# Optimization experiments

Hardware: AMD Instinct MI355X
Metric: run time of the kernel (lower is better)

Reference implementation:

```python
import jax, jax.numpy as jnp
import numpy as np

WS = 4      # window_size (RSUT5 default)
SHIFT = 2   # window_size // 2
NH = 8      # num_heads
DIM = 256
H0 = W0 = T0 = 32
B0 = 1


def _ln(x, g, b, eps=1e-5):
    m = x.mean(-1, keepdims=True)
    v = ((x - m) ** 2).mean(-1, keepdims=True)
    return (x - m) / jnp.sqrt(v + eps) * g + b


def _rel_index(ws):
    c = np.stack(np.meshgrid(np.arange(ws), np.arange(ws), np.arange(ws), indexing='ij')).reshape(3, -1)
    r = (c[:, :, None] - c[:, None, :]).transpose(1, 2, 0) + (ws - 1)
    return jnp.asarray((r[..., 0] * (2 * ws - 1) + r[..., 1]) * (2 * ws - 1) + r[..., 2])


def _partition(x, ws):
    B, H, W, T, C = x.shape
    x = x.reshape(B, H // ws, ws, W // ws, ws, T // ws, ws, C)
    return x.transpose(0, 1, 3, 5, 2, 4, 6, 7).reshape(-1, ws ** 3, C)


def _reverse(w, ws, B, H, W, T):
    C = w.shape[-1]
    x = w.reshape(B, H // ws, W // ws, T // ws, ws, ws, ws, C)
    return x.transpose(0, 1, 4, 2, 5, 3, 6, 7).reshape(B, H, W, T, C)


def _attn_mask(H, W, T, ws, ss):
    # static (numpy) replica of Block.createmask; H,W,T divisible by ws here
    img = np.zeros((H, W, T), np.float32)
    sls = (slice(0, -ws), slice(-ws, -ss), slice(-ss, None))
    cnt = 0
    for h in sls:
        for w in sls:
            for t in sls:
                img[h, w, t] = cnt
                cnt += 1
    mw = img.reshape(H // ws, ws, W // ws, ws, T // ws, ws).transpose(0, 2, 4, 1, 3, 5).reshape(-1, ws ** 3)
    d = mw[:, None, :] - mw[:, :, None]
    return jnp.asarray(np.where(d != 0, -100.0, 0.0).astype(np.float32))


def _swin(x, H, W, T, shift, mask, n1g, n1b, qkvw, qkvb, rpb, projw, projb, n2g, n2b, fc1w, fc1b, fc2w, fc2b):
    B, L, C = x.shape
    N = WS ** 3
    hd = C // NH
    shortcut = x
    x = _ln(x, n1g, n1b).reshape(B, H, W, T, C)
    if shift:
        x = jnp.roll(x, (-shift, -shift, -shift), axis=(1, 2, 3))
    xw = _partition(x, WS)                                        # [B*nW, N, C]
    qkv = (xw @ qkvw.T + qkvb).reshape(-1, N, 3, NH, hd).transpose(2, 0, 3, 1, 4)
    q, k, v = qkv[0], qkv[1], qkv[2]                              # [B*nW, NH, N, hd]
    attn = jnp.einsum('bhnd,bhmd->bhnm', q * (hd ** -0.5), k)
    attn = attn + rpb[_rel_index(WS)].transpose(2, 0, 1)[None]    # relative position bias
    if mask is not None:
        nW = mask.shape[0]
        attn = (attn.reshape(B, nW, NH, N, N) + mask[None, :, None]).reshape(-1, NH, N, N)
    attn = jax.nn.softmax(attn, axis=-1)
    out = jnp.einsum('bhnm,bhmd->bhnd', attn, v).transpose(0, 2, 1, 3).reshape(-1, N, C)
    out = out @ projw.T + projb
    x = _reverse(out, WS, B, H, W, T)
    if shift:
        x = jnp.roll(x, (shift, shift, shift), axis=(1, 2, 3))
    x = shortcut + x.reshape(B, L, C)
    h = _ln(x, n2g, n2b)
    h = jax.nn.gelu(h @ fc1w.T + fc1b, approximate=False) @ fc2w.T + fc2b
    return x + h


def setup_inputs() -> dict:
    key = jax.random.key(0)
    ks = iter(jax.random.split(key, 16))
    def rn(shape, s=0.02):
        return jax.random.normal(next(ks), shape, jnp.float32) * s
    d = {'x': jax.random.normal(next(ks), (B0, H0 * W0 * T0, DIM), jnp.float32),
         'H': H0, 'W': W0, 'T': T0,
         'norm_g': jnp.ones((DIM,), jnp.float32), 'norm_b': jnp.zeros((DIM,), jnp.float32)}
    for p in ('w', 's'):
        d[p + 'n1g'] = jnp.ones((DIM,), jnp.float32); d[p + 'n1b'] = jnp.zeros((DIM,), jnp.float32)
        d[p + 'qkvw'] = rn((3 * DIM, DIM)); d[p + 'qkvb'] = jnp.zeros((3 * DIM,), jnp.float32)
        d[p + 'rpb'] = rn(((2 * WS - 1) ** 3, NH))
        d[p + 'projw'] = rn((DIM, DIM)); d[p + 'projb'] = jnp.zeros((DIM,), jnp.float32)
        d[p + 'n2g'] = jnp.ones((DIM,), jnp.float32); d[p + 'n2b'] = jnp.zeros((DIM,), jnp.float32)
        d[p + 'fc1w'] = rn((4 * DIM, DIM)); d[p + 'fc1b'] = jnp.zeros((4 * DIM,), jnp.float32)
        d[p + 'fc2w'] = rn((DIM, 4 * DIM)); d[p + 'fc2b'] = jnp.zeros((DIM,), jnp.float32)
    return d


def reference(x, H, W, T, norm_g, norm_b,
              wn1g, wn1b, wqkvw, wqkvb, wrpb, wprojw, wprojb, wn2g, wn2b, wfc1w, wfc1b, wfc2w, wfc2b,
              sn1g, sn1b, sqkvw, sqkvb, srpb, sprojw, sprojb, sn2g, sn2b, sfc1w, sfc1b, sfc2w, sfc2b):
    mask = _attn_mask(H, W, T, WS, SHIFT)
    x = _swin(x, H, W, T, 0, None, wn1g, wn1b, wqkvw, wqkvb, wrpb, wprojw, wprojb, wn2g, wn2b, wfc1w, wfc1b, wfc2w, wfc2b)
    x = _swin(x, H, W, T, SHIFT, mask, sn1g, sn1b, sqkvw, sqkvb, srpb, sprojw, sprojb, sn2g, sn2b, sfc1w, sfc1b, sfc2w, sfc2b)
    B, L, C = x.shape
    # Block.norm + toConv: [B, L, C] -> [B, C, H, W, T]
    return _ln(x, norm_g, norm_b).reshape(B, H, W, T, C).transpose(0, 4, 1, 2, 3)
```

## Files before the change

kernel.cpp:

```cpp
#include <hip/hip_runtime.h>

typedef unsigned short u16;
typedef unsigned int   u32;
typedef __bf16 bfx8 __attribute__((ext_vector_type(8)));
typedef float  fx4  __attribute__((ext_vector_type(4)));

__device__ __forceinline__ u16 f2b(float f) {
    union { float f; u32 i; } v; v.f = f;
    u32 r = (v.i + 0x7fffu + ((v.i >> 16) & 1u)) >> 16;
    return (u16)r;
}
__device__ __forceinline__ u32 pk(float a, float b) {
    return (u32)f2b(a) | ((u32)f2b(b) << 16);
}
__device__ __forceinline__ float gelu(float x) {
    float u = 0.7978845608028654f * x * (1.0f + 0.044715f * x * x);
    float e = __expf(2.0f * u);
    float t = 1.0f - 2.0f / (e + 1.0f);
    return 0.5f * x * (1.0f + t);
}

__device__ __forceinline__ void gl2lds16(const u16* g, u16* l) {
    __builtin_amdgcn_global_load_lds(
        (const __attribute__((address_space(1))) u32*)(const void*)g,
        (__attribute__((address_space(3))) u32*)(void*)l, 16, 0, 0);
}

__device__ __forceinline__ int map_token(int r, int shift) {
    int win = r >> 6, n = r & 63;
    int wh = win >> 6, ww = (win >> 3) & 7, wt = win & 7;
    int h = wh * 4 + (n >> 4);
    int w = ww * 4 + ((n >> 2) & 3);
    int t = wt * 4 + (n & 3);
    h = (h + shift) & 31; w = (w + shift) & 31; t = (t + shift) & 31;
    return (h << 10) | (w << 5) | t;
}

struct CvtArgs { const float* src[8]; int cum[9]; };
__global__ __launch_bounds__(256) void cvt_kernel(CvtArgs a, u16* __restrict__ dst) {
    int g = (blockIdx.x * 256 + threadIdx.x) * 4;
    int t = 0;
    #pragma unroll
    for (int i = 1; i < 8; i++) t += (g >= a.cum[i]);
    int local = g - a.cum[t];
    float4 f = *(const float4*)(a.src[t] + local);
    uint2 o; o.x = pk(f.x, f.y); o.y = pk(f.z, f.w);
    *(uint2*)(dst + g) = o;
}

__global__ __launch_bounds__(64) void bias_kernel(const float* __restrict__ rpbW, const float* __restrict__ rpbS,
                                                  float* __restrict__ tab) {
    int bx = blockIdx.x;
    int shifted = bx >= 8;
    int idx = shifted ? bx - 8 : bx;
    int cls = shifted ? (idx >> 3) : 0;
    int head = idx & 7;
    const float* rpb = shifted ? rpbS : rpbW;
    float* out = tab + (size_t)bx * 4096;
    int i = threadIdx.x;
    int ih = i >> 4, iw = (i >> 2) & 3, it = i & 3;
    int mh = (cls >> 2) & 1, mw = (cls >> 1) & 1, mt = cls & 1;
    int labn = (mh ? (1 + (ih >> 1)) : 0) * 9 + (mw ? (1 + (iw >> 1)) : 0) * 3 + (mt ? (1 + (it >> 1)) : 0);
    for (int j = 0; j < 64; j++) {
        int jh = j >> 4, jw = (j >> 2) & 3, jt = j & 3;
        float v = rpb[(((ih - jh + 3) * 7 + (iw - jw + 3)) * 7 + (it - jt + 3)) * 8 + head];
        int labm = (mh ? (1 + (jh >> 1)) : 0) * 9 + (mw ? (1 + (jw >> 1)) : 0) * 3 + (mt ? (1 + (jt >> 1)) : 0);
        if (labm != labn) v -= 100.0f;
        out[i * 64 + j] = v;
    }
}

template<int GATHER, int F32OUT>
__global__ __launch_bounds__(256) void ln_kernel(const float* __restrict__ resid,
                                                 const float* __restrict__ g, const float* __restrict__ b,
                                                 void* __restrict__ outp, int shift) {
    int lane = threadIdx.x & 63;
    int row  = blockIdx.x * 4 + (threadIdx.x >> 6);
    int src  = GATHER ? map_token(row, shift) : row;
    float4 x = ((const float4*)(resid + src * 256))[lane];
    float s1 = x.x + x.y + x.z + x.w;
    float s2 = x.x * x.x + x.y * x.y + x.z * x.z + x.w * x.w;
    #pragma unroll
    for (int off = 1; off < 64; off <<= 1) { s1 += __shfl_xor(s1, off); s2 += __shfl_xor(s2, off); }
    float mean = s1 * (1.0f / 256.0f);
    float var  = s2 * (1.0f / 256.0f) - mean * mean;
    float rstd = rsqrtf(var + 1e-5f);
    int c = lane * 4;
    float4 gv = *(const float4*)(g + c);
    float4 bv = *(const float4*)(b + c);
    float y0 = (x.x - mean) * rstd * gv.x + bv.x;
    float y1 = (x.y - mean) * rstd * gv.y + bv.y;
    float y2 = (x.z - mean) * rstd * gv.z + bv.z;
    float y3 = (x.w - mean) * rstd * gv.w + bv.w;
    if (F32OUT) {
        float4 o; o.x = y0; o.y = y1; o.z = y2; o.w = y3;
        *(float4*)((float*)outp + row * 256 + c) = o;
    } else {
        uint2 o; o.x = pk(y0, y1); o.y = pk(y2, y3);
        *(uint2*)((u16*)outp + row * 256 + c) = o;
    }
}

template<int EPI>
__global__ __launch_bounds__(256) void gemm3(const u16* __restrict__ A, const u16* __restrict__ W,
                                             const float* __restrict__ bias,
                                             u16* __restrict__ outb, float* __restrict__ resid,
                                             int Nout, int K, int shift) {
    __shared__ u16 As[128 * 64];
    __shared__ u16 Bs[128 * 64];
    int lane = threadIdx.x & 63, w = threadIdx.x >> 6;
    int wm = w >> 1, wn = w & 1;
    int m0 = blockIdx.x * 128, n0 = blockIdx.y * 128;
    int lr = lane & 15, q = lane >> 4;

    fx4 acc[4][4] = {};

    for (int kt = 0; kt < K; kt += 64) {
        __syncthreads();
        #pragma unroll
        for (int s = 0; s < 4; s++) {
            int p = (w * 4 + s) * 64 + lane;
            int row = p >> 3;
            int g = (lane & 7) ^ (row & 7);
            gl2lds16(A + (size_t)(m0 + row) * K + kt + g * 8, As + p * 8);
            gl2lds16(W + (size_t)(n0 + row) * K + kt + g * 8, Bs + p * 8);
        }
        __syncthreads();
        #pragma unroll
        for (int kk = 0; kk < 2; kk++) {
            bfx8 af[4], bfr[4];
            #pragma unroll
            for (int t = 0; t < 4; t++) {
                int ra = wm * 64 + t * 16 + lr;
                int pa = (q + 4 * kk) ^ (ra & 7);
                af[t] = *(const bfx8*)(As + ra * 64 + pa * 8);
                int rb2 = wn * 64 + t * 16 + lr;
                int pb = (q + 4 * kk) ^ (rb2 & 7);
                bfr[t] = *(const bfx8*)(Bs + rb2 * 64 + pb * 8);
            }
            #pragma unroll
            for (int i = 0; i < 4; i++)
                #pragma unroll
                for (int j = 0; j < 4; j++)
                    acc[i][j] = __builtin_amdgcn_mfma_f32_16x16x32_bf16(bfr[j], af[i], acc[i][j], 0, 0, 0);
        }
    }

    float4 bv[4];
    #pragma unroll
    for (int j = 0; j < 4; j++) bv[j] = *(const float4*)(bias + n0 + wn * 64 + j * 16 + q * 4);
    #pragma unroll
    for (int i = 0; i < 4; i++) {
        int gr = m0 + wm * 64 + i * 16 + lr;
        int orow = (EPI == 3) ? map_token(gr, shift) : gr;
        #pragma unroll
        for (int j = 0; j < 4; j++) {
            int gc = n0 + wn * 64 + j * 16 + q * 4;
            float v0 = acc[i][j][0] + bv[j].x;
            float v1 = acc[i][j][1] + bv[j].y;
            float v2 = acc[i][j][2] + bv[j].z;
            float v3 = acc[i][j][3] + bv[j].w;
            if (EPI == 0) {
                uint2 o; o.x = pk(v0, v1); o.y = pk(v2, v3);
                *(uint2*)(outb + (size_t)gr * Nout + gc) = o;
            } else if (EPI == 1) {
                uint2 o; o.x = pk(gelu(v0), gelu(v1)); o.y = pk(gelu(v2), gelu(v3));
                *(uint2*)(outb + (size_t)gr * Nout + gc) = o;
            } else {
                float4 rv = *(float4*)(resid + orow * 256 + gc);
                rv.x += v0; rv.y += v1; rv.z += v2; rv.w += v3;
                *(float4*)(resid + orow * 256 + gc) = rv;
            }
        }
    }
}

__global__ __launch_bounds__(128) void attn3(const u16* __restrict__ qkv, const float* __restrict__ tab,
                                             u16* __restrict__ outb, int masked) {
    __shared__ u16 Pl[2][64][72];
    __shared__ u16 VT[2][32][72];
    int w = threadIdx.x >> 6, lane = threadIdx.x & 63;
    int id = blockIdx.x * 2 + w;
    int win = id >> 3, head = id & 7;
    int lr = lane & 15, q = lane >> 4;
    const u16* base = qkv + (size_t)win * 64 * 768 + head * 32;

    bfx8 qf[4], kf[4];
    #pragma unroll
    for (int t = 0; t < 4; t++) {
        const u16* rq = base + (lr + 16 * t) * 768 + q * 8;
        qf[t] = *(const bfx8*)(rq);
        kf[t] = *(const bfx8*)(rq + 256);
    }
    {
        const u16* rv = base + lane * 768 + 512;
        #pragma unroll
        for (int c = 0; c < 32; c += 8) {
            bfx8 vv = *(const bfx8*)(rv + c);
            #pragma unroll
            for (int j = 0; j < 8; j++) VT[w][c + j][lane] = ((const u16*)&vv)[j];
        }
    }

    fx4 sT[4][4] = {};
    #pragma unroll
    for (int jt = 0; jt < 4; jt++)
        #pragma unroll
        for (int it = 0; it < 4; it++)
            sT[jt][it] = __builtin_amdgcn_mfma_f32_16x16x32_bf16(kf[jt], qf[it], sT[jt][it], 0, 0, 0);

    int wh = win >> 6, ww = (win >> 3) & 7, wt = win & 7;
    int slab = masked ? (8 + ((((wh == 7) ? 4 : 0) | ((ww == 7) ? 2 : 0) | ((wt == 7) ? 1 : 0)) * 8) + head)
                      : head;
    const float* bt = tab + (size_t)slab * 4096 + q * 4;
    const float scale = 0.17677669529663687f;

    #pragma unroll
    for (int it = 0; it < 4; it++) {
        int i = lr + 16 * it;
        const float* br = bt + i * 64;
        float sv[4][4];
        float mx = -1e30f;
        #pragma unroll
        for (int jt = 0; jt < 4; jt++) {
            float4 bb = *(const float4*)(br + 16 * jt);
            sv[jt][0] = sT[jt][it][0] * scale + bb.x;
            sv[jt][1] = sT[jt][it][1] * scale + bb.y;
            sv[jt][2] = sT[jt][it][2] * scale + bb.z;
            sv[jt][3] = sT[jt][it][3] * scale + bb.w;
            mx = fmaxf(mx, fmaxf(fmaxf(sv[jt][0], sv[jt][1]), fmaxf(sv[jt][2], sv[jt][3])));
        }
        mx = fmaxf(mx, __shfl_xor(mx, 16));
        mx = fmaxf(mx, __shfl_xor(mx, 32));
        float sum = 0.f;
        #pragma unroll
        for (int jt = 0; jt < 4; jt++)
            #pragma unroll
            for (int r = 0; r < 4; r++) { sv[jt][r] = __expf(sv[jt][r] - mx); sum += sv[jt][r]; }
        sum += __shfl_xor(sum, 16);
        sum += __shfl_xor(sum, 32);
        float inv = 1.0f / sum;
        #pragma unroll
        for (int jt = 0; jt < 4; jt++) {
            uint2 pw;
            pw.x = pk(sv[jt][0] * inv, sv[jt][1] * inv);
            pw.y = pk(sv[jt][2] * inv, sv[jt][3] * inv);
            *(uint2*)&Pl[w][i][q * 4 + 16 * jt] = pw;
        }
    }

    fx4 o[4][2] = {};
    #pragma unroll
    for (int kk = 0; kk < 2; kk++) {
        bfx8 pf[4], vf[2];
        #pragma unroll
        for (int it = 0; it < 4; it++) pf[it] = *(const bfx8*)&Pl[w][lr + 16 * it][q * 8 + 32 * kk];
        #pragma unroll
        for (int dt = 0; dt < 2; dt++) vf[dt] = *(const bfx8*)&VT[w][lr + 16 * dt][q * 8 + 32 * kk];
        #pragma unroll
        for (int it = 0; it < 4; it++)
            #pragma unroll
            for (int dt = 0; dt < 2; dt++)
                o[it][dt] = __builtin_amdgcn_mfma_f32_16x16x32_bf16(vf[dt], pf[it], o[it][dt], 0, 0, 0);
    }

    u16* ob = outb + (size_t)win * 64 * 256 + head * 32;
    #pragma unroll
    for (int it = 0; it < 4; it++) {
        int i = lr + 16 * it;
        #pragma unroll
        for (int dt = 0; dt < 2; dt++) {
            uint2 ov;
            ov.x = pk(o[it][dt][0], o[it][dt][1]);
            ov.y = pk(o[it][dt][2], o[it][dt][3]);
            *(uint2*)(ob + i * 256 + dt * 16 + q * 4) = ov;
        }
    }
}

__global__ __launch_bounds__(256) void transpose_f32(const float* __restrict__ in, float* __restrict__ out) {
    __shared__ float tile[64][65];
    int t0 = blockIdx.x * 64;
    int c0 = blockIdx.y * 64;
    int row = threadIdx.x >> 2, cg = (threadIdx.x & 3) * 16;
    const float* src = in + (t0 + row) * 256 + c0 + cg;
    #pragma unroll
    for (int j = 0; j < 16; j += 4) {
        float4 v = *(const float4*)(src + j);
        tile[row][cg + j] = v.x; tile[row][cg + j + 1] = v.y;
        tile[row][cg + j + 2] = v.z; tile[row][cg + j + 3] = v.w;
    }
    __syncthreads();
    float tmp[16];
    #pragma unroll
    for (int j = 0; j < 16; j++) tmp[j] = tile[cg + j][row];
    float* dst = out + (c0 + row) * 32768 + t0 + cg;
    #pragma unroll
    for (int j = 0; j < 4; j++) *(float4*)(dst + 4 * j) = *(float4*)(tmp + 4 * j);
}

extern "C" void kernel_launch(void* const* d_in, const int* in_sizes, int n_in,
                              void* d_out, int out_size, void* d_ws, size_t ws_size,
                              hipStream_t stream) {
    const float* x      = (const float*)d_in[0];
    const float* norm_g = (const float*)d_in[4];
    const float* norm_b = (const float*)d_in[5];

    char* wsb = (char*)d_ws;
    float* resid = (float*)wsb;
    u16*   xn    = (u16*)(wsb + (size_t)32 * 1024 * 1024);
    u16*   big   = (u16*)(wsb + (size_t)48 * 1024 * 1024);
    u16*   attnb = (u16*)(wsb + (size_t)96 * 1024 * 1024);
    u16*   wb    = (u16*)(wsb + (size_t)112 * 1024 * 1024);
    float* tab   = (float*)(wsb + (size_t)115 * 1024 * 1024);
    float* xnf   = (float*)(wsb + (size_t)48 * 1024 * 1024);

    CvtArgs ca;
    static const int offs[9] = {0, 196608, 262144, 524288, 786432, 983040, 1048576, 1310720, 1572864};
    for (int i = 0; i < 9; i++) ca.cum[i] = offs[i];
    ca.src[0] = (const float*)d_in[6 + 2];
    ca.src[1] = (const float*)d_in[6 + 5];
    ca.src[2] = (const float*)d_in[6 + 9];
    ca.src[3] = (const float*)d_in[6 + 11];
    ca.src[4] = (const float*)d_in[19 + 2];
    ca.src[5] = (const float*)d_in[19 + 5];
    ca.src[6] = (const float*)d_in[19 + 9];
    ca.src[7] = (const float*)d_in[19 + 11];
    cvt_kernel<<<1536, 256, 0, stream>>>(ca, wb);
    bias_kernel<<<72, 64, 0, stream>>>((const float*)d_in[6 + 4], (const float*)d_in[19 + 4], tab);

    hipMemcpyAsync(resid, x, (size_t)32768 * 256 * 4, hipMemcpyDeviceToDevice, stream);

    for (int blk = 0; blk < 2; blk++) {
        void* const* P = d_in + 6 + blk * 13;
        const float* n1g  = (const float*)P[0];
        const float* n1b  = (const float*)P[1];
        const float* qkvb = (const float*)P[3];
        const float* pjb  = (const float*)P[6];
        const float* n2g  = (const float*)P[7];
        const float* n2b  = (const float*)P[8];
        const float* f1b  = (const float*)P[10];
        const float* f2b_ = (const float*)P[12];
        const u16* qkvw = wb + offs[0] + blk * 786432;
        const u16* pjw  = wb + offs[1] + blk * 786432;
        const u16* f1w  = wb + offs[2] + blk * 786432;
        const u16* f2w  = wb + offs[3] + blk * 786432;
        int shift = blk ? 2 : 0;

        ln_kernel<1, 0><<<8192, 256, 0, stream>>>(resid, n1g, n1b, xn, shift);
        gemm3<0><<<dim3(256, 6), 256, 0, stream>>>(xn, qkvw, qkvb, big, nullptr, 768, 256, 0);
        attn3<<<2048, 128, 0, stream>>>(big, tab, attnb, blk);
        gemm3<3><<<dim3(256, 2), 256, 0, stream>>>(attnb, pjw, pjb, nullptr, resid, 256, 256, shift);
        ln_kernel<0, 0><<<8192, 256, 0, stream>>>(resid, n2g, n2b, xn, 0);
        gemm3<1><<<dim3(256, 8), 256, 0, stream>>>(xn, f1w, f1b, big, nullptr, 1024, 256, 0);
        gemm3<2><<<dim3(256, 2), 256, 0, stream>>>(big, f2w, f2b_, nullptr, resid, 256, 1024, 0);
    }

    ln_kernel<0, 1><<<8192, 256, 0, stream>>>(resid, norm_g, norm_b, xnf, 0);
    transpose_f32<<<dim3(512, 4), 256, 0, stream>>>(xnf, (float*)d_out);
}
```

Measured before the change: 545.9 us.

## Retile GEMM to 256x128 blocks with K-step 32 and per-wave full-N tiles

Replaces the 128x128 GEMM tile (2x2 waves, K-step 64) with a 256x128 tile where each wave owns 64 rows by all 128 columns, using a K-step of 32 and a new LDS swizzle. B fragments are loaded once per k-step and reused across four A fragments, and launch bounds ask for two blocks per CU. The aim is more MFMA work per LDS read and less redundant loading of B. In exchange it uses 128 accumulator registers per thread, which risks spills or lower occupancy, and halves the grid, so fewer blocks are available to fill the CUs.

Result: slower. 560.2 us (+2.6%).

```diff
diff --git a/kernel.cpp b/kernel.cpp
--- a/kernel.cpp
+++ b/kernel.cpp
@@ -102,60 +102,60 @@
 }
 
 template<int EPI>
-__global__ __launch_bounds__(256) void gemm3(const u16* __restrict__ A, const u16* __restrict__ W,
-                                             const float* __restrict__ bias,
-                                             u16* __restrict__ outb, float* __restrict__ resid,
-                                             int Nout, int K, int shift) {
-    __shared__ u16 As[128 * 64];
-    __shared__ u16 Bs[128 * 64];
-    int lane = threadIdx.x & 63, w = threadIdx.x >> 6;
-    int wm = w >> 1, wn = w & 1;
-    int m0 = blockIdx.x * 128, n0 = blockIdx.y * 128;
+__global__ __launch_bounds__(256, 2) void gemm4(const u16* __restrict__ A, const u16* __restrict__ W,
+                                                const float* __restrict__ bias,
+                                                u16* __restrict__ outb, float* __restrict__ resid,
+                                                int Nout, int K, int shift) {
+    __shared__ u16 As[256 * 32];
+    __shared__ u16 Bs[128 * 32];
+    int tid = threadIdx.x;
+    int lane = tid & 63, w = tid >> 6;
+    int m0 = blockIdx.x * 256, n0 = blockIdx.y * 128;
     int lr = lane & 15, q = lane >> 4;
-
-    fx4 acc[4][4] = {};
-
-    for (int kt = 0; kt < K; kt += 64) {
+    int sw = q ^ ((lr >> 1) & 3);
+
+    fx4 acc[4][8] = {};
+
+    for (int kt = 0; kt < K; kt += 32) {
         __syncthreads();
         #pragma unroll
         for (int s = 0; s < 4; s++) {
-            int p = (w * 4 + s) * 64 + lane;
-            int row = p >> 3;
-            int g = (lane & 7) ^ (row & 7);
-            gl2lds16(A + (size_t)(m0 + row) * K + kt + g * 8, As + p * 8);
-            gl2lds16(W + (size_t)(n0 + row) * K + kt + g * 8, Bs + p * 8);
+            int sl = s * 256 + tid;
+            int row = sl >> 2;
+            int kg = (sl & 3) ^ ((row >> 1) & 3);
+            gl2lds16(A + (size_t)(m0 + row) * K + kt + kg * 8, As + sl * 8);
+        }
+        #pragma unroll
+        for (int s = 0; s < 2; s++) {
+            int sl = s * 256 + tid;
+            int row = sl >> 2;
+            int kg = (sl & 3) ^ ((row >> 1) & 3);
+            gl2lds16(W + (size_t)(n0 + row) * K + kt + kg * 8, Bs + sl * 8);
         }
         __syncthreads();
-        #pragma unroll
-        for (int kk = 0; kk < 2; kk++) {
-            bfx8 af[4], bfr[4];
+        bfx8 bfr[8];
+        #pragma unroll
+        for (int j = 0; j < 8; j++)
+            bfr[j] = *(const bfx8*)(Bs + ((j * 16 + lr) * 4 + sw) * 8);
+        #pragma unroll
+        for (int i = 0; i < 4; i++) {
+            bfx8 af = *(const bfx8*)(As + ((w * 64 + i * 16 + lr) * 4 + sw) * 8);
             #pragma unroll
-            for (int t = 0; t < 4; t++) {
-                int ra = wm * 64 + t * 16 + lr;
-                int pa = (q + 4 * kk) ^ (ra & 7);
-                af[t] = *(const bfx8*)(As + ra * 64 + pa * 8);
-                int rb2 = wn * 64 + t * 16 + lr;
-                int pb = (q + 4 * kk) ^ (rb2 & 7);
-                bfr[t] = *(const bfx8*)(Bs + rb2 * 64 + pb * 8);
-            }
-            #pragma unroll
-            for (int i = 0; i < 4; i++)
-                #pragma unroll
-                for (int j = 0; j < 4; j++)
-                    acc[i][j] = __builtin_amdgcn_mfma_f32_16x16x32_bf16(bfr[j], af[i], acc[i][j], 0, 0, 0);
-        }
-    }
-
-    float4 bv[4];
-    #pragma unroll
-    for (int j = 0; j < 4; j++) bv[j] = *(const float4*)(bias + n0 + wn * 64 + j * 16 + q * 4);
+            for (int j = 0; j < 8; j++)
+                acc[i][j] = __builtin_amdgcn_mfma_f32_16x16x32_bf16(bfr[j], af, acc[i][j], 0, 0, 0);
+        }
+    }
+
+    float4 bv[8];
+    #pragma unroll
+    for (int j = 0; j < 8; j++) bv[j] = *(const float4*)(bias + n0 + j * 16 + q * 4);
     #pragma unroll
     for (int i = 0; i < 4; i++) {
-        int gr = m0 + wm * 64 + i * 16 + lr;
+        int gr = m0 + w * 64 + i * 16 + lr;
         int orow = (EPI == 3) ? map_token(gr, shift) : gr;
         #pragma unroll
-        for (int j = 0; j < 4; j++) {
-            int gc = n0 + wn * 64 + j * 16 + q * 4;
+        for (int j = 0; j < 8; j++) {
+            int gc = n0 + j * 16 + q * 4;
             float v0 = acc[i][j][0] + bv[j].x;
             float v1 = acc[i][j][1] + bv[j].y;
             float v2 = acc[i][j][2] + bv[j].z;
@@ -348,12 +348,12 @@
         int shift = blk ? 2 : 0;
 
         ln_kernel<1, 0><<<8192, 256, 0, stream>>>(resid, n1g, n1b, xn, shift);
-        gemm3<0><<<dim3(256, 6), 256, 0, stream>>>(xn, qkvw, qkvb, big, nullptr, 768, 256, 0);
+        gemm4<0><<<dim3(128, 6), 256, 0, stream>>>(xn, qkvw, qkvb, big, nullptr, 768, 256, 0);
         attn3<<<2048, 128, 0, stream>>>(big, tab, attnb, blk);
-        gemm3<3><<<dim3(256, 2), 256, 0, stream>>>(attnb, pjw, pjb, nullptr, resid, 256, 256, shift);
+        gemm4<3><<<dim3(128, 2), 256, 0, stream>>>(attnb, pjw, pjb, nullptr, resid, 256, 256, shift);
         ln_kernel<0, 0><<<8192, 256, 0, stream>>>(resid, n2g, n2b, xn, 0);
-        gemm3<1><<<dim3(256, 8), 256, 0, stream>>>(xn, f1w, f1b, big, nullptr, 1024, 256, 0);
-        gemm3<2><<<dim3(256, 2), 256, 0, stream>>>(big, f2w, f2b_, nullptr, resid, 256, 1024, 0);
+        gemm4<1><<<dim3(128, 8), 256, 0, stream>>>(xn, f1w, f1b, big, nullptr, 1024, 256, 0);
+        gemm4<2><<<dim3(128, 2), 256, 0, stream>>>(big, f2w, f2b_, nullptr, resid, 256, 1024, 0);
     }
 
     ln_kernel<0, 1><<<8192, 256, 0, stream>>>(resid, norm_g, norm_b, xnf, 0);
```

## Halve GEMM K-tile with precomputed load pointers and drop residual copy

Applied to the files above, without the earlier changes.

The GEMM now stages 32-wide K tiles instead of 64, using fixed per-thread global and LDS pointers and a simpler swizzle, which halves shared memory per block and cuts index arithmetic. The initial device-to-device copy of x into the residual buffer is removed: block 0's LayerNorm reads x directly, and the projection epilogue writes x plus the projection output into the residual buffer. Smaller K tiles double the number of barriers per GEMM and give fewer MFMAs per sync, in exchange for possible higher occupancy.

Measured after the change: 534.5 us. 1.02x faster.

```diff
diff --git a/kernel.cpp b/kernel.cpp
--- a/kernel.cpp
+++ b/kernel.cpp
@@ -102,48 +102,53 @@
 }
 
 template<int EPI>
-__global__ __launch_bounds__(256) void gemm3(const u16* __restrict__ A, const u16* __restrict__ W,
+__global__ __launch_bounds__(256) void gemm5(const u16* __restrict__ A, const u16* __restrict__ W,
                                              const float* __restrict__ bias,
                                              u16* __restrict__ outb, float* __restrict__ resid,
+                                             const float* __restrict__ xin,
                                              int Nout, int K, int shift) {
-    __shared__ u16 As[128 * 64];
-    __shared__ u16 Bs[128 * 64];
-    int lane = threadIdx.x & 63, w = threadIdx.x >> 6;
+    __shared__ u16 As[128 * 32];
+    __shared__ u16 Bs[128 * 32];
+    int tid = threadIdx.x;
+    int lane = tid & 63, w = tid >> 6;
     int wm = w >> 1, wn = w & 1;
     int m0 = blockIdx.x * 128, n0 = blockIdx.y * 128;
     int lr = lane & 15, q = lane >> 4;
+    int sw = q ^ ((lr >> 1) & 3);
+
+    int s0 = tid, s1 = 256 + tid;
+    int r0 = s0 >> 2, r1 = s1 >> 2;
+    int k0 = (s0 & 3) ^ ((r0 >> 1) & 3);
+    int k1 = (s1 & 3) ^ ((r1 >> 1) & 3);
+    const u16* ga0 = A + (size_t)(m0 + r0) * K + k0 * 8;
+    const u16* ga1 = A + (size_t)(m0 + r1) * K + k1 * 8;
+    const u16* gb0 = W + (size_t)(n0 + r0) * K + k0 * 8;
+    const u16* gb1 = W + (size_t)(n0 + r1) * K + k1 * 8;
+    u16* la0 = As + s0 * 8; u16* la1 = As + s1 * 8;
+    u16* lb0 = Bs + s0 * 8; u16* lb1 = Bs + s1 * 8;
+
+    const u16* rdA = As + (wm * 64 + lr) * 32 + sw * 8;
+    const u16* rdB = Bs + (wn * 64 + lr) * 32 + sw * 8;
 
     fx4 acc[4][4] = {};
 
-    for (int kt = 0; kt < K; kt += 64) {
+    for (int kt = 0; kt < K; kt += 32) {
         __syncthreads();
-        #pragma unroll
-        for (int s = 0; s < 4; s++) {
-            int p = (w * 4 + s) * 64 + lane;
-            int row = p >> 3;
-            int g = (lane & 7) ^ (row & 7);
-            gl2lds16(A + (size_t)(m0 + row) * K + kt + g * 8, As + p * 8);
-            gl2lds16(W + (size_t)(n0 + row) * K + kt + g * 8, Bs + p * 8);
-        }
+        gl2lds16(ga0, la0); gl2lds16(ga1, la1);
+        gl2lds16(gb0, lb0); gl2lds16(gb1, lb1);
+        ga0 += 32; ga1 += 32; gb0 += 32; gb1 += 32;
         __syncthreads();
-        #pragma unroll
-        for (int kk = 0; kk < 2; kk++) {
-            bfx8 af[4], bfr[4];
+        bfx8 af[4], bfr[4];
+        #pragma unroll
+        for (int t = 0; t < 4; t++) {
+            af[t]  = *(const bfx8*)(rdA + t * 512);
+            bfr[t] = *(const bfx8*)(rdB + t * 512);
+        }
+        #pragma unroll
+        for (int i = 0; i < 4; i++)
             #pragma unroll
-            for (int t = 0; t < 4; t++) {
-                int ra = wm * 64 + t * 16 + lr;
-                int pa = (q + 4 * kk) ^ (ra & 7);
-                af[t] = *(const bfx8*)(As + ra * 64 + pa * 8);
-                int rb2 = wn * 64 + t * 16 + lr;
-                int pb = (q + 4 * kk) ^ (rb2 & 7);
-                bfr[t] = *(const bfx8*)(Bs + rb2 * 64 + pb * 8);
-            }
-            #pragma unroll
-            for (int i = 0; i < 4; i++)
-                #pragma unroll
-                for (int j = 0; j < 4; j++)
-                    acc[i][j] = __builtin_amdgcn_mfma_f32_16x16x32_bf16(bfr[j], af[i], acc[i][j], 0, 0, 0);
-        }
+            for (int j = 0; j < 4; j++)
+                acc[i][j] = __builtin_amdgcn_mfma_f32_16x16x32_bf16(bfr[j], af[i], acc[i][j], 0, 0, 0);
     }
 
     float4 bv[4];
@@ -152,7 +157,7 @@
     #pragma unroll
     for (int i = 0; i < 4; i++) {
         int gr = m0 + wm * 64 + i * 16 + lr;
-        int orow = (EPI == 3) ? map_token(gr, shift) : gr;
+        int orow = (EPI >= 3) ? map_token(gr, shift) : gr;
         #pragma unroll
         for (int j = 0; j < 4; j++) {
             int gc = n0 + wn * 64 + j * 16 + q * 4;
@@ -166,6 +171,11 @@
             } else if (EPI == 1) {
                 uint2 o; o.x = pk(gelu(v0), gelu(v1)); o.y = pk(gelu(v2), gelu(v3));
                 *(uint2*)(outb + (size_t)gr * Nout + gc) = o;
+            } else if (EPI == 4) {
+                float4 xv = *(const float4*)(xin + orow * 256 + gc);
+                float4 rv;
+                rv.x = xv.x + v0; rv.y = xv.y + v1; rv.z = xv.z + v2; rv.w = xv.w + v3;
+                *(float4*)(resid + orow * 256 + gc) = rv;
             } else {
                 float4 rv = *(float4*)(resid + orow * 256 + gc);
                 rv.x += v0; rv.y += v1; rv.z += v2; rv.w += v3;
@@ -328,8 +338,6 @@
     ca.src[7] = (const float*)d_in[19 + 11];
     cvt_kernel<<<1536, 256, 0, stream>>>(ca, wb);
     bias_kernel<<<72, 64, 0, stream>>>((const float*)d_in[6 + 4], (const float*)d_in[19 + 4], tab);
-
-    hipMemcpyAsync(resid, x, (size_t)32768 * 256 * 4, hipMemcpyDeviceToDevice, stream);
 
     for (int blk = 0; blk < 2; blk++) {
         void* const* P = d_in + 6 + blk * 13;
@@ -346,14 +354,18 @@
         const u16* f1w  = wb + offs[2] + blk * 786432;
         const u16* f2w  = wb + offs[3] + blk * 786432;
         int shift = blk ? 2 : 0;
-
-        ln_kernel<1, 0><<<8192, 256, 0, stream>>>(resid, n1g, n1b, xn, shift);
-        gemm3<0><<<dim3(256, 6), 256, 0, stream>>>(xn, qkvw, qkvb, big, nullptr, 768, 256, 0);
+        const float* ln1src = blk ? resid : x;
+
+        ln_kernel<1, 0><<<8192, 256, 0, stream>>>(ln1src, n1g, n1b, xn, shift);
+        gemm5<0><<<dim3(256, 6), 256, 0, stream>>>(xn, qkvw, qkvb, big, nullptr, nullptr, 768, 256, 0);
         attn3<<<2048, 128, 0, stream>>>(big, tab, attnb, blk);
-        gemm3<3><<<dim3(256, 2), 256, 0, stream>>>(attnb, pjw, pjb, nullptr, resid, 256, 256, shift);
+        if (blk == 0)
+            gemm5<4><<<dim3(256, 2), 256, 0, stream>>>(attnb, pjw, pjb, nullptr, resid, x, 256, 256, 0);
+        else
+            gemm5<3><<<dim3(256, 2), 256, 0, stream>>>(attnb, pjw, pjb, nullptr, resid, nullptr, 256, 256, shift);
         ln_kernel<0, 0><<<8192, 256, 0, stream>>>(resid, n2g, n2b, xn, 0);
-        gemm3<1><<<dim3(256, 8), 256, 0, stream>>>(xn, f1w, f1b, big, nullptr, 1024, 256, 0);
-        gemm3<2><<<dim3(256, 2), 256, 0, stream>>>(big, f2w, f2b_, nullptr, resid, 256, 1024, 0);
+        gemm5<1><<<dim3(256, 8), 256, 0, stream>>>(xn, f1w, f1b, big, nullptr, nullptr, 1024, 256, 0);
+        gemm5<2><<<dim3(256, 2), 256, 0, stream>>>(big, f2w, f2b_, nullptr, resid, nullptr, 256, 1024, 0);
     }
 
     ln_kernel<0, 1><<<8192, 256, 0, stream>>>(resid, norm_g, norm_b, xnf, 0);
```
